# Kernel optimization log

Hardware: AMD Instinct MI355X
Metric: run time of the kernel (lower is better)

Reference implementation:

```python
import jax, jax.numpy as jnp
import numpy as np

N_NODES = 100000
N_EDGES = 1600000
IN_CH = 128
OUT_CH = 128

def setup_inputs() -> dict:
    key = jax.random.key(0)
    k1, k2, k3, k4, k5 = jax.random.split(key, 5)
    x = jax.random.normal(k1, (N_NODES, IN_CH), dtype=jnp.float32)
    src = jax.random.randint(k2, (N_EDGES,), 0, N_NODES, dtype=jnp.int64)
    dst = jax.random.randint(k3, (N_EDGES,), 0, N_NODES, dtype=jnp.int64)
    edge_index = jnp.stack([src, dst], axis=0)
    W = jax.random.normal(k4, (OUT_CH, IN_CH), dtype=jnp.float32) * (1.0 / np.sqrt(IN_CH))
    b = jax.random.normal(k5, (OUT_CH,), dtype=jnp.float32) * 0.01
    return {"x": x, "edge_index": edge_index, "W": W, "b": b}

def reference(x, edge_index, W, b):
    n = x.shape[0]
    src, dst = edge_index[0], edge_index[1]
    loop = jnp.arange(n, dtype=edge_index.dtype)
    src_all = jnp.concatenate([src, loop])  # [E+N]
    dst_all = jnp.concatenate([dst, loop])  # [E+N]
    # in-degree (with self loops) per node
    deg = jax.ops.segment_sum(jnp.ones_like(dst_all, dtype=x.dtype), dst_all, num_segments=n)
    norm = (deg[src_all] * deg[dst_all]) ** -0.5
    norm = jnp.where(jnp.isinf(norm), 0.0, norm)
    h = x @ W.T + b  # [N, out_ch]
    msg = h[src_all] * norm[:, None]  # [E+N, out_ch]
    out = jax.ops.segment_sum(msg, dst_all, num_segments=n)  # [N, out_ch]
    return out
```

## Files before the change

### kernel.cpp

```cpp
#include <hip/hip_runtime.h>
#include <hip/hip_bf16.h>


#define N_NODES 100000
#define N_EDGES 1600000
#define CH 128
#define NC 49
#define NBLKA 782
#define CAPB 80
#define BPU 46
#define NCHUNK 17
#define NFB 1563
#define FCAP 1280
#define STCAP 2560

using bf16x8 = __attribute__((ext_vector_type(8))) short;
using f32x4  = __attribute__((ext_vector_type(4))) float;

__device__ inline unsigned short f2bf(float f) {
    unsigned u = __float_as_uint(f);
    u += 0x7fffu + ((u >> 16) & 1u);
    return (unsigned short)(u >> 16);
}
__device__ inline float bflo(unsigned u) { return __uint_as_float(u << 16); }
__device__ inline float bfhi(unsigned u) { return __uint_as_float(u & 0xffff0000u); }

__global__ __launch_bounds__(256) void k_place(const int* __restrict__ src,
                                               const int* __restrict__ dst,
                                               int* __restrict__ cntG,
                                               unsigned* __restrict__ E1,
                                               int* __restrict__ ftail) {
    __shared__ int hist[NC];
    __shared__ int boff[NC + 1];
    __shared__ int cur[NC];
    __shared__ unsigned stage[2048];
    const int t    = threadIdx.x;
    const int bid  = blockIdx.x;
    const int base = bid * 2048;
    const int n    = min(2048, N_EDGES - base);

    { int i = bid * 256 + t; if (i < 1600) ftail[i] = 0; }
    if (t < NC) hist[t] = 0;
    __syncthreads();

    int s[8], d[8];
#pragma unroll
    for (int h = 0; h < 2; ++h) {
        int idx = h * 1024 + 4 * t;
        if (idx < n) {
            int4 sv = *(const int4*)&src[base + idx];
            int4 dv = *(const int4*)&dst[base + idx];
            s[4*h+0] = sv.x; s[4*h+1] = sv.y; s[4*h+2] = sv.z; s[4*h+3] = sv.w;
            d[4*h+0] = dv.x; d[4*h+1] = dv.y; d[4*h+2] = dv.z; d[4*h+3] = dv.w;
        } else {
            d[4*h+0] = d[4*h+1] = d[4*h+2] = d[4*h+3] = -1;
            s[4*h+0] = s[4*h+1] = s[4*h+2] = s[4*h+3] = 0;
        }
    }
#pragma unroll
    for (int j = 0; j < 8; ++j)
        if (d[j] >= 0) atomicAdd(&hist[d[j] >> 11], 1);
    __syncthreads();

    if (t == 0) {
        int run = 0;
        for (int k = 0; k < NC; ++k) { boff[k] = run; run += hist[k]; }
        boff[NC] = run;
    }
    __syncthreads();
    if (t < NC) cur[t] = boff[t];
    __syncthreads();

#pragma unroll
    for (int j = 0; j < 8; ++j)
        if (d[j] >= 0) {
            int k = d[j] >> 11;
            int pos = atomicAdd(&cur[k], 1);
            stage[pos] = ((unsigned)s[j] << 11) | (unsigned)(d[j] & 2047);
        }
    __syncthreads();

    if (t < NC) cntG[(size_t)t * NBLKA + bid] = min(hist[t], CAPB);

    const int tot = boff[NC];
    for (int i = t; i < tot; i += 256) {
        int lo = 0, hi = NC;
#pragma unroll
        for (int it = 0; it < 6; ++it) {
            int mid = (lo + hi) >> 1;
            bool c = (boff[mid] <= i);
            lo = c ? mid : lo;
            hi = c ? hi : mid;
        }
        int p = i - boff[lo];
        if (p < CAPB)
            E1[((size_t)lo * NBLKA + bid) * CAPB + p] = stage[i];
    }
}

__global__ __launch_bounds__(256) void k_sortB(const unsigned* __restrict__ E1,
                                               const int* __restrict__ cntG,
                                               int* __restrict__ ftail,
                                               unsigned* __restrict__ E2) {
    __shared__ int hist[32];
    __shared__ int boff[33];
    __shared__ int cur[32];
    __shared__ int gb[32];
    __shared__ int cnt[BPU];
    __shared__ unsigned stage[STCAP];
    const int cb  = blockIdx.x / NCHUNK;
    const int u   = blockIdx.x % NCHUNK;
    const int sb0 = u * BPU;
    const int t   = threadIdx.x;

    if (t < 32) hist[t] = 0;
    if (t < BPU) cnt[t] = cntG[(size_t)cb * NBLKA + sb0 + t];
    __syncthreads();

    const unsigned* e1 = E1 + ((size_t)cb * NBLKA + sb0) * CAPB;

    for (int i = t; i < BPU * CAPB; i += 256) {
        int sb = i / CAPB, sl = i - sb * CAPB;
        if (sl < cnt[sb]) atomicAdd(&hist[(e1[i] >> 6) & 31], 1);
    }
    __syncthreads();

    if (t < 32) gb[t] = atomicAdd(&ftail[cb * 32 + t], hist[t]);
    if (t == 0) {
        int run = 0;
        for (int k = 0; k < 32; ++k) { boff[k] = run; run += hist[k]; }
        boff[32] = run;
    }
    __syncthreads();
    if (t < 32) cur[t] = boff[t];
    __syncthreads();

    for (int i = t; i < BPU * CAPB; i += 256) {
        int sb = i / CAPB, sl = i - sb * CAPB;
        if (sl < cnt[sb]) {
            unsigned v = e1[i];
            int k = (v >> 6) & 31;
            int pos = atomicAdd(&cur[k], 1);
            if (pos < STCAP)
                stage[pos] = ((v >> 11) << 6) | (v & 63);
        }
    }
    __syncthreads();

    const int tot = min(boff[32], STCAP);
    for (int i = t; i < tot; i += 256) {
        int lo = 0, hi = 32;
#pragma unroll
        for (int it = 0; it < 5; ++it) {
            int mid = (lo + hi) >> 1;
            bool c = (boff[mid] <= i);
            lo = c ? mid : lo;
            hi = c ? hi : mid;
        }
        int p = gb[lo] + (i - boff[lo]);
        int fb = cb * 32 + lo;
        if (p < FCAP) E2[(size_t)fb * FCAP + p] = stage[i];
    }
}

__device__ inline void cvt8(const float4 a, const float4 b, bf16x8& h, bf16x8& l) {
    bf16x8 H, L;
#define CV(i, f) { unsigned short hb = f2bf(f); H[i] = (short)hb;               \
                   L[i] = (short)f2bf((f) - __uint_as_float((unsigned)hb << 16)); }
    CV(0, a.x) CV(1, a.y) CV(2, a.z) CV(3, a.w)
    CV(4, b.x) CV(5, b.y) CV(6, b.z) CV(7, b.w)
#undef CV
    h = H; l = L;
}

#define MFMA(a, b, c) __builtin_amdgcn_mfma_f32_16x16x32_bf16((a), (b), (c), 0, 0, 0)

__global__ __launch_bounds__(256) void k_gemm(const float* __restrict__ x,
                                              const float* __restrict__ W,
                                              const float* __restrict__ b,
                                              const unsigned* __restrict__ E2,
                                              const int* __restrict__ ftail,
                                              unsigned short* __restrict__ hs) {
    __shared__ __align__(16) unsigned short wh[CH * CH];
    __shared__ __align__(16) unsigned short wl[CH * CH];
    const int t = threadIdx.x;
    const int lane = t & 63;
    const int l15  = lane & 15;
    const int lhi  = lane >> 4;

    int* dbin = (int*)wh;
    if (t < 128) dbin[t] = 0;
    __syncthreads();
    {
        const int fb0 = blockIdx.x * 2;
        int n0 = ftail[fb0]; if (n0 > FCAP) n0 = FCAP;
        const unsigned* e0 = E2 + (size_t)fb0 * FCAP;
        for (int i = t; i < n0; i += 256) atomicAdd(&dbin[e0[i] & 63], 1);
        const int fb1 = fb0 + 1;
        if (fb1 < NFB) {
            int n1 = ftail[fb1]; if (n1 > FCAP) n1 = FCAP;
            const unsigned* e1p = E2 + (size_t)fb1 * FCAP;
            for (int i = t; i < n1; i += 256) atomicAdd(&dbin[64 + (e1p[i] & 63)], 1);
        }
    }
    __syncthreads();
    float rreg[2][4];
#pragma unroll
    for (int rf = 0; rf < 2; ++rf) {
        int lb = (t >> 6) * 32 + rf * 16 + lhi * 4;
#pragma unroll
        for (int j = 0; j < 4; ++j)
            rreg[rf][j] = rsqrtf((float)(dbin[lb + j] + 1));
    }
    __syncthreads();

    for (int c = t; c < 2048; c += 256) {
        int o   = c >> 4;
        int kk  = (c & 15) << 3;
        const float* wp = &W[(size_t)o * CH + kk];
        float4 w0 = *(const float4*)wp;
        float4 w1 = *(const float4*)(wp + 4);
        bf16x8 H, L;
        cvt8(w0, w1, H, L);
        unsigned boff = ((unsigned)((o << 8) | (kk << 1))) ^ ((unsigned)(o & 7) << 4);
        *(bf16x8*)((char*)wh + boff) = H;
        *(bf16x8*)((char*)wl + boff) = L;
    }
    __syncthreads();

    const int kc = lhi << 3;
    const int row_base = blockIdx.x * 128 + (t >> 6) * 32;

    int r0 = row_base + l15;       if (r0 > N_NODES - 1) r0 = N_NODES - 1;
    int r1 = row_base + 16 + l15;  if (r1 > N_NODES - 1) r1 = N_NODES - 1;
    const float* x0 = &x[(size_t)r0 * CH + kc];
    const float* x1 = &x[(size_t)r1 * CH + kc];

    float4 xa[4][2], xb[4][2];
#pragma unroll
    for (int ks = 0; ks < 4; ++ks) {
        xa[ks][0] = *(const float4*)(x0 + ks * 32);
        xa[ks][1] = *(const float4*)(x0 + ks * 32 + 4);
        xb[ks][0] = *(const float4*)(x1 + ks * 32);
        xb[ks][1] = *(const float4*)(x1 + ks * 32 + 4);
    }

    f32x4 acc[2][8];
#pragma unroll
    for (int rf = 0; rf < 2; ++rf)
#pragma unroll
        for (int cf = 0; cf < 8; ++cf)
            acc[rf][cf] = (f32x4){0.f, 0.f, 0.f, 0.f};

#pragma unroll
    for (int ks = 0; ks < 4; ++ks) {
        bf16x8 ah0, al0, ah1, al1;
        cvt8(xa[ks][0], xa[ks][1], ah0, al0);
        cvt8(xb[ks][0], xb[ks][1], ah1, al1);
        const unsigned kb = (unsigned)((ks * 32 + kc) << 1);
#pragma unroll
        for (int cf = 0; cf < 8; ++cf) {
            int o = cf * 16 + l15;
            unsigned boff = (((unsigned)(o << 8)) + kb) ^ ((unsigned)(o & 7) << 4);
            bf16x8 bh = *(const bf16x8*)((const char*)wh + boff);
            bf16x8 bl = *(const bf16x8*)((const char*)wl + boff);
            acc[0][cf] = MFMA(ah0, bh, acc[0][cf]);
            acc[1][cf] = MFMA(ah1, bh, acc[1][cf]);
            acc[0][cf] = MFMA(al0, bh, acc[0][cf]);
            acc[1][cf] = MFMA(al1, bh, acc[1][cf]);
            acc[0][cf] = MFMA(ah0, bl, acc[0][cf]);
            acc[1][cf] = MFMA(ah1, bl, acc[1][cf]);
        }
    }

    float bcol[8];
#pragma unroll
    for (int cf = 0; cf < 8; ++cf) bcol[cf] = b[cf * 16 + l15];

#pragma unroll
    for (int rf = 0; rf < 2; ++rf) {
        int rb = row_base + rf * 16 + lhi * 4;
        if (rb >= N_NODES) continue;
#pragma unroll
        for (int j = 0; j < 4; ++j) {
            size_t ro = (size_t)(rb + j) * CH;
            float ri = rreg[rf][j];
#pragma unroll
            for (int cf = 0; cf < 8; ++cf)
                hs[ro + cf * 16 + l15] = f2bf(ri * (acc[rf][cf][j] + bcol[cf]));
        }
    }
}

#define ACC8(u)                                                            \
    do {                                                                   \
        acc[0] += bflo((u).x); acc[1] += bfhi((u).x);                      \
        acc[2] += bflo((u).y); acc[3] += bfhi((u).y);                      \
        acc[4] += bflo((u).z); acc[5] += bfhi((u).z);                      \
        acc[6] += bflo((u).w); acc[7] += bfhi((u).w);                      \
    } while (0)

__global__ __launch_bounds__(256) void k_spmm(const unsigned* __restrict__ E2,
                                              const int* __restrict__ ftail,
                                              const unsigned short* __restrict__ hs,
                                              float* __restrict__ out) {
    __shared__ int bins[64];
    __shared__ int boff[65];
    __shared__ int cur[64];
    __shared__ int srt[FCAP];
    const int fb    = blockIdx.x;
    const int node0 = fb * 64;
    const int t     = threadIdx.x;
    const unsigned* e2 = E2 + (size_t)fb * FCAP;
    const uint4* hp = (const uint4*)hs;

    if (t < 64) bins[t] = 0;
    int n = ftail[fb]; if (n > FCAP) n = FCAP;
    __syncthreads();

    for (int i = t; i < n; i += 256) atomicAdd(&bins[e2[i] & 63], 1);
    __syncthreads();

    if (t == 0) {
        int run = 0;
        for (int k = 0; k < 64; ++k) { boff[k] = run; run += bins[k]; }
        boff[64] = run;
    }
    __syncthreads();
    if (t < 64) cur[t] = boff[t];
    __syncthreads();

    for (int i = t; i < n; i += 256) {
        unsigned v = e2[i];
        int pos = atomicAdd(&cur[v & 63], 1);
        srt[pos] = (int)(v >> 6);
    }
    __syncthreads();

    const int grp  = t >> 4;
    const int lane = t & 15;
#pragma unroll
    for (int r = 0; r < 4; ++r) {
        const int nl   = grp * 4 + r;
        const int node = node0 + nl;
        if (node >= N_NODES) continue;
        float acc[8] = {};
        {
            uint4 u = hp[(size_t)node * 16 + lane];
            ACC8(u);
        }
        int e  = boff[nl];
        int e1 = boff[nl + 1];
        for (; e + 8 <= e1; e += 8) {
            int s0 = srt[e + 0], s1 = srt[e + 1], s2 = srt[e + 2], s3 = srt[e + 3];
            int s4 = srt[e + 4], s5 = srt[e + 5], s6 = srt[e + 6], s7 = srt[e + 7];
            uint4 u0 = hp[(size_t)s0 * 16 + lane];
            uint4 u1 = hp[(size_t)s1 * 16 + lane];
            uint4 u2 = hp[(size_t)s2 * 16 + lane];
            uint4 u3 = hp[(size_t)s3 * 16 + lane];
            uint4 u4 = hp[(size_t)s4 * 16 + lane];
            uint4 u5 = hp[(size_t)s5 * 16 + lane];
            uint4 u6 = hp[(size_t)s6 * 16 + lane];
            uint4 u7 = hp[(size_t)s7 * 16 + lane];
            ACC8(u0); ACC8(u1); ACC8(u2); ACC8(u3);
            ACC8(u4); ACC8(u5); ACC8(u6); ACC8(u7);
        }
        for (; e + 4 <= e1; e += 4) {
            int s0 = srt[e + 0];
            int s1 = srt[e + 1];
            int s2 = srt[e + 2];
            int s3 = srt[e + 3];
            uint4 u0 = hp[(size_t)s0 * 16 + lane];
            uint4 u1 = hp[(size_t)s1 * 16 + lane];
            uint4 u2 = hp[(size_t)s2 * 16 + lane];
            uint4 u3 = hp[(size_t)s3 * 16 + lane];
            ACC8(u0); ACC8(u1); ACC8(u2); ACC8(u3);
        }
        for (; e < e1; ++e) {
            uint4 u = hp[(size_t)srt[e] * 16 + lane];
            ACC8(u);
        }
        float ri = rsqrtf((float)(bins[nl] + 1));
        f32x4 o0, o1;
        o0[0] = ri * acc[0]; o0[1] = ri * acc[1]; o0[2] = ri * acc[2]; o0[3] = ri * acc[3];
        o1[0] = ri * acc[4]; o1[1] = ri * acc[5]; o1[2] = ri * acc[6]; o1[3] = ri * acc[7];
        *(f32x4*)&out[(size_t)node * CH + lane * 8]     = o0;
        *(f32x4*)&out[(size_t)node * CH + lane * 8 + 4] = o1;
    }
}

extern "C" void kernel_launch(void* const* d_in, const int* in_sizes, int n_in,
                              void* d_out, int out_size, void* d_ws, size_t ws_size,
                              hipStream_t stream) {
    const float* x  = (const float*)d_in[0];
    const int*   ei = (const int*)d_in[1];
    const float* W  = (const float*)d_in[2];
    const float* b  = (const float*)d_in[3];
    float* out = (float*)d_out;

    const int* src = (const int*)ei;
    const int* dst = (const int*)ei + N_EDGES;

    int*      ftail = (int*)d_ws;
    int*      cntG  = ftail + 1600;
    unsigned* E2    = (unsigned*)(cntG + 38336);
    unsigned short* hs = (unsigned short*)(E2 + (size_t)NFB * FCAP);
    unsigned* E1    = (unsigned*)hs;

    k_place<<<NBLKA, 256, 0, stream>>>(src, dst, cntG, E1, ftail);
    k_sortB<<<NC * NCHUNK, 256, 0, stream>>>(E1, cntG, ftail, E2);
    k_gemm<<<NBLKA, 256, 0, stream>>>(x, W, b, E2, ftail, hs);
    k_spmm<<<NFB, 256, 0, stream>>>(E2, ftail, hs, out);
}
```

Baseline: 223.0 us.

## Halve edges per placement block, parallelize prefix scans, split spmm launch

The edge-placement kernel now handles 1024 edges per block instead of 2048, doubling the block count and shrinking per-block capacities (CAPB, BPU, STCAP), and the sort stage is regridded to match. The serial single-thread prefix sums in k_place and k_sortB are replaced with wavefront shuffle scans. The spmm launch is split into two launches using a block offset parameter. The intent is more parallelism and less serial latency in the preprocessing kernels. The risks are extra launch overhead and overflow of the tighter per-bucket capacities.

```diff
diff --git a/kernel.cpp b/kernel.cpp
--- a/kernel.cpp
+++ b/kernel.cpp
@@ -6,13 +6,14 @@
 #define N_EDGES 1600000
 #define CH 128
 #define NC 49
-#define NBLKA 782
-#define CAPB 80
-#define BPU 46
-#define NCHUNK 17
+#define EPB 1024
+#define NBLKA 1563
+#define CAPB 48
+#define BPU 23
+#define NCHB 68
 #define NFB 1563
 #define FCAP 1280
-#define STCAP 2560
+#define STCAP 768
 
 using bf16x8 = __attribute__((ext_vector_type(8))) short;
 using f32x4  = __attribute__((ext_vector_type(4))) float;
@@ -33,46 +34,50 @@
     __shared__ int hist[NC];
     __shared__ int boff[NC + 1];
     __shared__ int cur[NC];
-    __shared__ unsigned stage[2048];
+    __shared__ unsigned stage[EPB];
     const int t    = threadIdx.x;
     const int bid  = blockIdx.x;
-    const int base = bid * 2048;
-    const int n    = min(2048, N_EDGES - base);
-
-    { int i = bid * 256 + t; if (i < 1600) ftail[i] = 0; }
+    const int base = bid * EPB;
+    const int n    = min(EPB, N_EDGES - base);
+
+    if (t < 2) { int i = bid * 2 + t; if (i < 1600) ftail[i] = 0; }
     if (t < NC) hist[t] = 0;
     __syncthreads();
 
-    int s[8], d[8];
-#pragma unroll
-    for (int h = 0; h < 2; ++h) {
-        int idx = h * 1024 + 4 * t;
+    int s[4], d[4];
+    {
+        int idx = 4 * t;
         if (idx < n) {
             int4 sv = *(const int4*)&src[base + idx];
             int4 dv = *(const int4*)&dst[base + idx];
-            s[4*h+0] = sv.x; s[4*h+1] = sv.y; s[4*h+2] = sv.z; s[4*h+3] = sv.w;
-            d[4*h+0] = dv.x; d[4*h+1] = dv.y; d[4*h+2] = dv.z; d[4*h+3] = dv.w;
+            s[0] = sv.x; s[1] = sv.y; s[2] = sv.z; s[3] = sv.w;
+            d[0] = dv.x; d[1] = dv.y; d[2] = dv.z; d[3] = dv.w;
         } else {
-            d[4*h+0] = d[4*h+1] = d[4*h+2] = d[4*h+3] = -1;
-            s[4*h+0] = s[4*h+1] = s[4*h+2] = s[4*h+3] = 0;
-        }
-    }
-#pragma unroll
-    for (int j = 0; j < 8; ++j)
+            d[0] = d[1] = d[2] = d[3] = -1;
+            s[0] = s[1] = s[2] = s[3] = 0;
+        }
+    }
+#pragma unroll
+    for (int j = 0; j < 4; ++j)
         if (d[j] >= 0) atomicAdd(&hist[d[j] >> 11], 1);
     __syncthreads();
 
-    if (t == 0) {
-        int run = 0;
-        for (int k = 0; k < NC; ++k) { boff[k] = run; run += hist[k]; }
-        boff[NC] = run;
+    if (t < 64) {
+        int v = (t < NC) ? hist[t] : 0;
+#pragma unroll
+        for (int off = 1; off < 64; off <<= 1) {
+            int u = __shfl_up(v, off, 64);
+            if (t >= off) v += u;
+        }
+        if (t < NC) boff[t + 1] = v;
+        if (t == 0) boff[0] = 0;
     }
     __syncthreads();
     if (t < NC) cur[t] = boff[t];
     __syncthreads();
 
 #pragma unroll
-    for (int j = 0; j < 8; ++j)
+    for (int j = 0; j < 4; ++j)
         if (d[j] >= 0) {
             int k = d[j] >> 11;
             int pos = atomicAdd(&cur[k], 1);
@@ -108,13 +113,16 @@
     __shared__ int gb[32];
     __shared__ int cnt[BPU];
     __shared__ unsigned stage[STCAP];
-    const int cb  = blockIdx.x / NCHUNK;
-    const int u   = blockIdx.x % NCHUNK;
+    const int cb  = blockIdx.x / NCHB;
+    const int u   = blockIdx.x % NCHB;
     const int sb0 = u * BPU;
     const int t   = threadIdx.x;
 
     if (t < 32) hist[t] = 0;
-    if (t < BPU) cnt[t] = cntG[(size_t)cb * NBLKA + sb0 + t];
+    if (t < BPU) {
+        int sb = sb0 + t;
+        cnt[t] = (sb < NBLKA) ? cntG[(size_t)cb * NBLKA + sb] : 0;
+    }
     __syncthreads();
 
     const unsigned* e1 = E1 + ((size_t)cb * NBLKA + sb0) * CAPB;
@@ -126,10 +134,15 @@
     __syncthreads();
 
     if (t < 32) gb[t] = atomicAdd(&ftail[cb * 32 + t], hist[t]);
-    if (t == 0) {
-        int run = 0;
-        for (int k = 0; k < 32; ++k) { boff[k] = run; run += hist[k]; }
-        boff[32] = run;
+    if (t < 64) {
+        int v = (t < 32) ? hist[t] : 0;
+#pragma unroll
+        for (int off = 1; off < 32; off <<= 1) {
+            int w = __shfl_up(v, off, 64);
+            if (t >= off) v += w;
+        }
+        if (t < 32) boff[t + 1] = v;
+        if (t == 0) boff[0] = 0;
     }
     __syncthreads();
     if (t < 32) cur[t] = boff[t];
@@ -303,12 +316,13 @@
 __global__ __launch_bounds__(256) void k_spmm(const unsigned* __restrict__ E2,
                                               const int* __restrict__ ftail,
                                               const unsigned short* __restrict__ hs,
-                                              float* __restrict__ out) {
+                                              float* __restrict__ out,
+                                              int fb0) {
     __shared__ int bins[64];
     __shared__ int boff[65];
     __shared__ int cur[64];
     __shared__ int srt[FCAP];
-    const int fb    = blockIdx.x;
+    const int fb    = blockIdx.x + fb0;
     const int node0 = fb * 64;
     const int t     = threadIdx.x;
     const unsigned* e2 = E2 + (size_t)fb * FCAP;
@@ -403,12 +417,13 @@
 
     int*      ftail = (int*)d_ws;
     int*      cntG  = ftail + 1600;
-    unsigned* E2    = (unsigned*)(cntG + 38336);
+    unsigned* E2    = (unsigned*)(cntG + 76608);
     unsigned short* hs = (unsigned short*)(E2 + (size_t)NFB * FCAP);
     unsigned* E1    = (unsigned*)hs;
 
     k_place<<<NBLKA, 256, 0, stream>>>(src, dst, cntG, E1, ftail);
-    k_sortB<<<NC * NCHUNK, 256, 0, stream>>>(E1, cntG, ftail, E2);
-    k_gemm<<<NBLKA, 256, 0, stream>>>(x, W, b, E2, ftail, hs);
-    k_spmm<<<NFB, 256, 0, stream>>>(E2, ftail, hs, out);
-}
+    k_sortB<<<NC * NCHB, 256, 0, stream>>>(E1, cntG, ftail, E2);
+    k_gemm<<<(N_NODES + 127) / 128, 256, 0, stream>>>(x, W, b, E2, ftail, hs);
+    k_spmm<<<782, 256, 0, stream>>>(E2, ftail, hs, out, 0);
+    k_spmm<<<NFB - 782, 256, 0, stream>>>(E2, ftail, hs, out, 782);
+}
```

Result: no change. 222.1 us (-0.4%).
